# Kernel tuning notes

Hardware: AMD Instinct MI355X
Metric: run time of the kernel (lower is better)

Reference implementation:

```python
import jax, jax.numpy as jnp
import numpy as np

B, H, OUT = 16384, 1024, 128
W_SCALE = 0.03  # ~1/sqrt(H) so attention logits / softmax stay well-conditioned


def setup_inputs() -> dict:
    key = jax.random.key(0)
    ks = jax.random.split(key, 12)
    return {
        "f1": jax.random.normal(ks[0], (B, H), jnp.float32),
        "f2": jax.random.normal(ks[1], (B, H), jnp.float32),
        "f3": jax.random.normal(ks[2], (B, H), jnp.float32),
        "f4": jax.random.normal(ks[3], (B, H), jnp.float32),
        "Wq": jax.random.normal(ks[4], (H, H), jnp.float32) * W_SCALE,
        "bq": jax.random.normal(ks[5], (H,), jnp.float32) * W_SCALE,
        "Wk": jax.random.normal(ks[6], (H, H), jnp.float32) * W_SCALE,
        "bk": jax.random.normal(ks[7], (H,), jnp.float32) * W_SCALE,
        "Wv": jax.random.normal(ks[8], (H, H), jnp.float32) * W_SCALE,
        "bv": jax.random.normal(ks[9], (H,), jnp.float32) * W_SCALE,
        "Wfc": jax.random.normal(ks[10], (H, OUT), jnp.float32) * W_SCALE,
        "bfc": jax.random.normal(ks[11], (OUT,), jnp.float32) * W_SCALE,
    }


def reference(f1, f2, f3, f4, Wq, bq, Wk, bk, Wv, bv, Wfc, bfc):
    # Stack the 4 backbone features: z [B, 4, H]
    z = jnp.stack([f1, f2, f3, f4], axis=1)
    q = z @ Wq + bq            # [B, 4, H]
    k = z @ Wk + bk            # [B, 4, H]
    v = z @ Wv + bv            # [B, 4, H]
    # Tiny 4x4 self-attention over the 4 model-feature tokens
    score = jax.nn.softmax(jnp.einsum('bth,bsh->bts', q, k), axis=-1)  # [B,4,4]
    att = jnp.einsum('bts,bsh->bth', score, v)                          # [B,4,H]
    x = jnp.sum(att, axis=1)                                            # [B,H]
    out = jax.nn.softmax(x @ Wfc + bfc, axis=-1)                        # [B,OUT]
    return (x, out)
```

## Files before the change

kernel.cpp:

```cpp
#include <hip/hip_runtime.h>
#include <hip/hip_bf16.h>
#include <stdint.h>

#define B_SZ 16384
#define H_SZ 1024
#define OUT_SZ 128

typedef __attribute__((ext_vector_type(4))) float f32x4;
typedef __attribute__((ext_vector_type(8))) _Float16 h16x8;
typedef unsigned short u16;
typedef unsigned int u32;

__device__ __forceinline__ u16 f2h(float f) {
  union { _Float16 h; u16 u; } v; v.h = (_Float16)f; return v.u;
}
__device__ __forceinline__ float h2f(u16 u) {
  union { u16 u; _Float16 h; } v; v.u = u; return (float)v.h;
}
__device__ __forceinline__ u32 pk2(float a, float b) {
  return (u32)f2h(a) | ((u32)f2h(b) << 16);
}

__device__ __forceinline__ void gl_lds16(const void* g, void* l) {
  __builtin_amdgcn_global_load_lds(
      (const __attribute__((address_space(1))) u32*)g,
      (__attribute__((address_space(3))) u32*)l, 16, 0, 0);
}

template<int MODE>
__global__ __launch_bounds__(256, 4) void gemm_nt(
    const u16* __restrict__ Aptr, const u16* __restrict__ Bptr,
    int N, int K,
    float* __restrict__ ep_f, u16* __restrict__ ep_b,
    const float* __restrict__ ep_v,
    const float* zf0, const float* zf1, const float* zf2, const float* zf3)
{
  constexpr int BM = 128, BN = 128, BK = 32;
  __shared__ __align__(16) u16 sA[BM * BK];
  __shared__ __align__(16) u16 sB[BN * BK];
  const int tid  = threadIdx.x;
  const int wave = tid >> 6;
  const int lane = tid & 63;
  const int qd   = lane >> 4;
  const int c16  = lane & 15;
  const int bm0  = blockIdx.x * BM;
  const int bn0  = blockIdx.y * BN;
  const int wm   = (wave >> 1) * 64;
  const int wn   = (wave & 1) * 64;
  const size_t FBS = (size_t)B_SZ * H_SZ;

  f32x4 acc[4][4];
#pragma unroll
  for (int i = 0; i < 4; ++i)
#pragma unroll
    for (int j = 0; j < 4; ++j)
      acc[i][j] = (f32x4){0.f, 0.f, 0.f, 0.f};

  for (int k0 = 0; k0 < K; k0 += BK) {
#pragma unroll
    for (int i = 0; i < 2; ++i) {
      int slot = tid + i * 256;
      int r = slot >> 2, pp = slot & 3;
      int cc = pp ^ ((r >> 1) & 3);
      {
        int gm = bm0 + r;
        const u16* gp;
        if (MODE == 1)
          gp = Aptr + (size_t)(gm & 3) * FBS + (size_t)(gm >> 2) * H_SZ + (k0 + cc * 8);
        else
          gp = Aptr + (size_t)gm * K + (k0 + cc * 8);
        gl_lds16(gp, &sA[(size_t)(slot & ~63) * 8]);
      }
      {
        int gn = bn0 + r;
        const u16* gp = Bptr + (size_t)gn * K + (k0 + cc * 8);
        gl_lds16(gp, &sB[(size_t)(slot & ~63) * 8]);
      }
    }
    __syncthreads();
    h16x8 af[4], bfr[4];
#pragma unroll
    for (int im = 0; im < 4; ++im) {
      int m = wm + im * 16 + c16;
      int slot = m * 4 + (qd ^ ((m >> 1) & 3));
      af[im] = *(const h16x8*)&sA[slot * 8];
    }
#pragma unroll
    for (int in = 0; in < 4; ++in) {
      int n = wn + in * 16 + c16;
      int slot = n * 4 + (qd ^ ((n >> 1) & 3));
      bfr[in] = *(const h16x8*)&sB[slot * 8];
    }
#pragma unroll
    for (int im = 0; im < 4; ++im)
#pragma unroll
      for (int in = 0; in < 4; ++in)
        acc[im][in] = __builtin_amdgcn_mfma_f32_16x16x32_f16(af[im], bfr[in], acc[im][in], 0, 0, 0);
    __syncthreads();
  }

  if constexpr (MODE == 0) {
#pragma unroll
    for (int im = 0; im < 4; ++im)
#pragma unroll
      for (int in = 0; in < 4; ++in) {
        int n = bn0 + wn + in * 16 + c16;
#pragma unroll
        for (int r = 0; r < 4; ++r) {
          int m = bm0 + wm + im * 16 + qd * 4 + r;
          ep_b[(size_t)m * N + n] = f2h(acc[im][in][r]);
        }
      }
  } else if constexpr (MODE == 1) {
    const float* zf[4] = {zf0, zf1, zf2, zf3};
#pragma unroll
    for (int im = 0; im < 4; ++im) {
      int mrow = bm0 + wm + im * 16 + qd * 4;
      size_t b = (size_t)(mrow >> 2);
      float p[4][4];
#pragma unroll
      for (int r = 0; r < 4; ++r)
#pragma unroll
        for (int s = 0; s < 4; ++s) p[r][s] = 0.f;
#pragma unroll
      for (int in = 0; in < 4; ++in) {
        int n = bn0 + wn + in * 16 + c16;
        float akv = ep_v[n];
        float rv[4];
#pragma unroll
        for (int r = 0; r < 4; ++r) rv[r] = acc[im][in][r] + akv;
#pragma unroll
        for (int s = 0; s < 4; ++s) {
          float zv = zf[s][b * H_SZ + n];
#pragma unroll
          for (int r = 0; r < 4; ++r) p[r][s] += rv[r] * zv;
        }
      }
#pragma unroll
      for (int r = 0; r < 4; ++r)
#pragma unroll
        for (int s = 0; s < 4; ++s) {
          float v = p[r][s];
          v += __shfl_xor(v, 1);
          v += __shfl_xor(v, 2);
          v += __shfl_xor(v, 4);
          v += __shfl_xor(v, 8);
          if (c16 == 0) atomicAdd(&ep_f[b * 16 + r * 4 + s], v);
        }
    }
  } else if constexpr (MODE == 2) {
#pragma unroll
    for (int im = 0; im < 4; ++im)
#pragma unroll
      for (int in = 0; in < 4; ++in) {
        int n = bn0 + wn + in * 16 + c16;
        float bvv = 4.0f * ep_v[n];
#pragma unroll
        for (int r = 0; r < 4; ++r) {
          int m = bm0 + wm + im * 16 + qd * 4 + r;
          float v = acc[im][in][r] + bvv;
          ep_f[(size_t)m * H_SZ + n] = v;
          ep_b[(size_t)m * H_SZ + n] = f2h(v);
        }
      }
  } else {
#pragma unroll
    for (int im = 0; im < 4; ++im)
#pragma unroll
      for (int in = 0; in < 4; ++in) {
        int n = bn0 + wn + in * 16 + c16;
        float bc = ep_v[n];
#pragma unroll
        for (int r = 0; r < 4; ++r) {
          int m = bm0 + wm + im * 16 + qd * 4 + r;
          ep_f[(size_t)m * N + n] = acc[im][in][r] + bc;
        }
      }
  }
}

__global__ __launch_bounds__(256) void prep_weights(
    const float* __restrict__ Wq, const float* __restrict__ Wk,
    const float* __restrict__ Wv, const float* __restrict__ Wfc,
    const float* __restrict__ bq,
    u16* __restrict__ Wq16, u16* __restrict__ Wk16,
    u16* __restrict__ WvT, u16* __restrict__ WfcT,
    float* __restrict__ ak)
{
  __shared__ float t[32][33];
  int blk = blockIdx.x, tid = threadIdx.x;
  if (blk < 2048) {
    const float* src = (blk < 1024) ? Wq : Wk;
    u16* dst = (blk < 1024) ? Wq16 : Wk16;
    size_t i0 = (size_t)(blk & 1023) * 1024 + tid * 4;
    float4 v = *(const float4*)(src + i0);
    *(uint2*)(dst + i0) = make_uint2(pk2(v.x, v.y), pk2(v.z, v.w));
  } else if (blk < 3200) {
    int lx = tid & 31, ly = tid >> 5;
    if (blk < 3072) {
      int ti = blk - 2048;
      int tx = ti & 31, ty = ti >> 5;
#pragma unroll
      for (int k = 0; k < 4; ++k)
        t[ly + 8 * k][lx] = Wv[(size_t)(ty * 32 + ly + 8 * k) * 1024 + tx * 32 + lx];
      __syncthreads();
#pragma unroll
      for (int k = 0; k < 4; ++k)
        WvT[(size_t)(tx * 32 + ly + 8 * k) * 1024 + ty * 32 + lx] = f2h(t[lx][ly + 8 * k]);
    } else {
      int ti = blk - 3072;
      int tx = ti & 3, ty = ti >> 2;
#pragma unroll
      for (int k = 0; k < 4; ++k)
        t[ly + 8 * k][lx] = Wfc[(size_t)(ty * 32 + ly + 8 * k) * 128 + tx * 32 + lx];
      __syncthreads();
#pragma unroll
      for (int k = 0; k < 4; ++k)
        WfcT[(size_t)(tx * 32 + ly + 8 * k) * 1024 + ty * 32 + lx] = f2h(t[lx][ly + 8 * k]);
    }
  } else {
    int wave = tid >> 6, lane = tid & 63;
    int row = (blk - 3200) * 4 + wave;
    float s = 0.f;
    for (int i = lane; i < 1024; i += 64)
      s += Wk[(size_t)row * 1024 + i] * bq[i];
#pragma unroll
    for (int m = 1; m < 64; m <<= 1) s += __shfl_xor(s, m);
    if (lane == 0) ak[row] = s;
  }
}

__global__ __launch_bounds__(256) void convert4(
    const float* __restrict__ f1, const float* __restrict__ f2,
    const float* __restrict__ f3, const float* __restrict__ f4,
    u16* __restrict__ Zh)
{
  int a = blockIdx.x >> 13;
  const float* f = (a == 0) ? f1 : (a == 1) ? f2 : (a == 2) ? f3 : f4;
  size_t off = (size_t)(blockIdx.x & 8191) * 2048 + threadIdx.x * 8;
  float4 v0 = *(const float4*)(f + off);
  float4 v1 = *(const float4*)(f + off + 4);
  *(uint4*)(Zh + (size_t)a * B_SZ * H_SZ + off) =
      make_uint4(pk2(v0.x, v0.y), pk2(v0.z, v0.w), pk2(v1.x, v1.y), pk2(v1.z, v1.w));
}

__global__ __launch_bounds__(256) void softmax_g(
    const float* __restrict__ logits, const u16* __restrict__ Zh,
    u16* __restrict__ G)
{
  const size_t FBS = (size_t)B_SZ * H_SZ;
  int wave = threadIdx.x >> 6, lane = threadIdx.x & 63;
  size_t b = (size_t)blockIdx.x * 4 + wave;
  float l[16];
#pragma unroll
  for (int i = 0; i < 16; ++i) l[i] = logits[b * 16 + i];
  float w0 = 0, w1 = 0, w2 = 0, w3 = 0;
#pragma unroll
  for (int t = 0; t < 4; ++t) {
    float a0 = l[t * 4], a1 = l[t * 4 + 1], a2 = l[t * 4 + 2], a3 = l[t * 4 + 3];
    float mx = fmaxf(fmaxf(a0, a1), fmaxf(a2, a3));
    float e0 = __expf(a0 - mx), e1 = __expf(a1 - mx), e2 = __expf(a2 - mx), e3 = __expf(a3 - mx);
    float inv = 1.0f / (e0 + e1 + e2 + e3);
    w0 += e0 * inv; w1 += e1 * inv; w2 += e2 * inv; w3 += e3 * inv;
  }
#pragma unroll
  for (int ch = 0; ch < 2; ++ch) {
    size_t h0 = (size_t)lane * 8 + ch * 512;
    float g[8];
#pragma unroll
    for (int j = 0; j < 8; ++j) g[j] = 0.f;
#pragma unroll
    for (int s = 0; s < 4; ++s) {
      float ws = (s == 0) ? w0 : (s == 1) ? w1 : (s == 2) ? w2 : w3;
      uint4 zz = *(const uint4*)(Zh + (size_t)s * FBS + b * H_SZ + h0);
      u32 zs[4] = {zz.x, zz.y, zz.z, zz.w};
#pragma unroll
      for (int j = 0; j < 4; ++j) {
        g[2 * j]     += ws * h2f((u16)(zs[j] & 0xffffu));
        g[2 * j + 1] += ws * h2f((u16)(zs[j] >> 16));
      }
    }
    *(uint4*)(G + b * H_SZ + h0) =
        make_uint4(pk2(g[0], g[1]), pk2(g[2], g[3]), pk2(g[4], g[5]), pk2(g[6], g[7]));
  }
}

__global__ __launch_bounds__(256) void softmax_out(
    const float* __restrict__ L2, float* __restrict__ out)
{
  int wave = threadIdx.x >> 6, lane = threadIdx.x & 63;
  size_t row = (size_t)blockIdx.x * 4 + wave;
  float2 v = *(const float2*)(L2 + row * 128 + lane * 2);
  float mx = fmaxf(v.x, v.y);
#pragma unroll
  for (int m = 1; m < 64; m <<= 1) mx = fmaxf(mx, __shfl_xor(mx, m));
  float e0 = __expf(v.x - mx), e1 = __expf(v.y - mx);
  float s = e0 + e1;
#pragma unroll
  for (int m = 1; m < 64; m <<= 1) s += __shfl_xor(s, m);
  float inv = 1.0f / s;
  *(float2*)(out + row * 128 + lane * 2) = make_float2(e0 * inv, e1 * inv);
}

extern "C" void kernel_launch(void* const* d_in, const int* in_sizes, int n_in,
                              void* d_out, int out_size, void* d_ws, size_t ws_size,
                              hipStream_t stream)
{
  const float* f1  = (const float*)d_in[0];
  const float* f2  = (const float*)d_in[1];
  const float* f3  = (const float*)d_in[2];
  const float* f4  = (const float*)d_in[3];
  const float* Wq  = (const float*)d_in[4];
  const float* bq  = (const float*)d_in[5];
  const float* Wk  = (const float*)d_in[6];
  const float* Wv  = (const float*)d_in[8];
  const float* bv  = (const float*)d_in[9];
  const float* Wfc = (const float*)d_in[10];
  const float* bfc = (const float*)d_in[11];

  float* x_out = (float*)d_out;
  float* out2  = x_out + (size_t)B_SZ * H_SZ;

  const size_t BH = (size_t)B_SZ * H_SZ;
  const size_t HH = (size_t)H_SZ * H_SZ;
  char* w = (char*)d_ws;
  u16* Zh   = (u16*)w;  w += 4 * BH * sizeof(u16);
  u16* G    = (u16*)w;  w += BH * sizeof(u16);
  u16* Xh   = (u16*)w;  w += BH * sizeof(u16);
  u16* Wq16 = (u16*)w;  w += HH * 2;
  u16* Wk16 = (u16*)w;  w += HH * 2;
  u16* AT   = (u16*)w;  w += HH * 2;
  u16* WvT  = (u16*)w;  w += HH * 2;
  u16* WfcT = (u16*)w;  w += (size_t)OUT_SZ * H_SZ * 2;
  float* ak     = (float*)w;  w += H_SZ * sizeof(float);
  float* logits = (float*)w;  w += (size_t)B_SZ * 16 * sizeof(float);
  float* fcl    = (float*)w;  w += (size_t)B_SZ * OUT_SZ * sizeof(float);

  hipMemsetAsync(logits, 0, (size_t)B_SZ * 16 * sizeof(float), stream);
  prep_weights<<<3456, 256, 0, stream>>>(Wq, Wk, Wv, Wfc, bq,
      Wq16, Wk16, WvT, WfcT, ak);
  convert4<<<32768, 256, 0, stream>>>(f1, f2, f3, f4, Zh);
  gemm_nt<0><<<dim3(8, 8), 256, 0, stream>>>(
      Wk16, Wq16, 1024, 1024, nullptr, AT, nullptr,
      nullptr, nullptr, nullptr, nullptr);
  gemm_nt<1><<<dim3(512, 8), 256, 0, stream>>>(
      Zh, AT, 1024, 1024, logits, nullptr, ak, f1, f2, f3, f4);
  softmax_g<<<4096, 256, 0, stream>>>(logits, Zh, G);
  gemm_nt<2><<<dim3(128, 8), 256, 0, stream>>>(
      G, WvT, 1024, 1024, x_out, Xh, bv,
      nullptr, nullptr, nullptr, nullptr);
  gemm_nt<3><<<dim3(128, 1), 256, 0, stream>>>(
      Xh, WfcT, 128, 1024, fcl, nullptr, bfc,
      nullptr, nullptr, nullptr, nullptr);
  softmax_out<<<4096, 256, 0, stream>>>(fcl, out2);
}
```

Measured before the change: 784.8 us.

## Double-buffer GEMM LDS tiles and replace logit atomics with partial-sum buffer

The GEMM main loop now uses two LDS buffers per operand, issuing the next K-tile's global-to-LDS loads before computing on the current tile, so load latency can overlap MFMA work. The logits epilogue no longer uses atomicAdd into a zeroed buffer. Each of the 16 column groups writes its partial sum to a separate slot in a scratch area that aliases Xh, and softmax_g reduces those partials with shuffles. This removes the memset and the atomic contention, but doubles LDS use, which may lower occupancy. It also relies on Xh being free until the later GEMM writes it.

New measurement: 695.6 us. 11.4% less time.

```diff
diff --git a/kernel.cpp b/kernel.cpp
--- a/kernel.cpp
+++ b/kernel.cpp
@@ -36,8 +36,8 @@
     const float* zf0, const float* zf1, const float* zf2, const float* zf3)
 {
   constexpr int BM = 128, BN = 128, BK = 32;
-  __shared__ __align__(16) u16 sA[BM * BK];
-  __shared__ __align__(16) u16 sB[BN * BK];
+  __shared__ __align__(16) u16 sA[2][BM * BK];
+  __shared__ __align__(16) u16 sB[2][BN * BK];
   const int tid  = threadIdx.x;
   const int wave = tid >> 6;
   const int lane = tid & 63;
@@ -49,14 +49,7 @@
   const int wn   = (wave & 1) * 64;
   const size_t FBS = (size_t)B_SZ * H_SZ;
 
-  f32x4 acc[4][4];
-#pragma unroll
-  for (int i = 0; i < 4; ++i)
-#pragma unroll
-    for (int j = 0; j < 4; ++j)
-      acc[i][j] = (f32x4){0.f, 0.f, 0.f, 0.f};
-
-  for (int k0 = 0; k0 < K; k0 += BK) {
+  auto stage = [&](int buf, int k0) {
 #pragma unroll
     for (int i = 0; i < 2; ++i) {
       int slot = tid + i * 256;
@@ -69,27 +62,40 @@
           gp = Aptr + (size_t)(gm & 3) * FBS + (size_t)(gm >> 2) * H_SZ + (k0 + cc * 8);
         else
           gp = Aptr + (size_t)gm * K + (k0 + cc * 8);
-        gl_lds16(gp, &sA[(size_t)(slot & ~63) * 8]);
+        gl_lds16(gp, &sA[buf][(size_t)(slot & ~63) * 8]);
       }
       {
         int gn = bn0 + r;
         const u16* gp = Bptr + (size_t)gn * K + (k0 + cc * 8);
-        gl_lds16(gp, &sB[(size_t)(slot & ~63) * 8]);
-      }
-    }
-    __syncthreads();
+        gl_lds16(gp, &sB[buf][(size_t)(slot & ~63) * 8]);
+      }
+    }
+  };
+
+  f32x4 acc[4][4];
+#pragma unroll
+  for (int i = 0; i < 4; ++i)
+#pragma unroll
+    for (int j = 0; j < 4; ++j)
+      acc[i][j] = (f32x4){0.f, 0.f, 0.f, 0.f};
+
+  stage(0, 0);
+  __syncthreads();
+  int cur = 0;
+  for (int k0 = 0; k0 < K; k0 += BK) {
+    if (k0 + BK < K) stage(cur ^ 1, k0 + BK);
     h16x8 af[4], bfr[4];
 #pragma unroll
     for (int im = 0; im < 4; ++im) {
       int m = wm + im * 16 + c16;
       int slot = m * 4 + (qd ^ ((m >> 1) & 3));
-      af[im] = *(const h16x8*)&sA[slot * 8];
+      af[im] = *(const h16x8*)&sA[cur][slot * 8];
     }
 #pragma unroll
     for (int in = 0; in < 4; ++in) {
       int n = wn + in * 16 + c16;
       int slot = n * 4 + (qd ^ ((n >> 1) & 3));
-      bfr[in] = *(const h16x8*)&sB[slot * 8];
+      bfr[in] = *(const h16x8*)&sB[cur][slot * 8];
     }
 #pragma unroll
     for (int im = 0; im < 4; ++im)
@@ -97,6 +103,7 @@
       for (int in = 0; in < 4; ++in)
         acc[im][in] = __builtin_amdgcn_mfma_f32_16x16x32_f16(af[im], bfr[in], acc[im][in], 0, 0, 0);
     __syncthreads();
+    cur ^= 1;
   }
 
   if constexpr (MODE == 0) {
@@ -113,6 +120,7 @@
       }
   } else if constexpr (MODE == 1) {
     const float* zf[4] = {zf0, zf1, zf2, zf3};
+    const int yg = (int)blockIdx.y * 2 + (wn >> 6);
 #pragma unroll
     for (int im = 0; im < 4; ++im) {
       int mrow = bm0 + wm + im * 16 + qd * 4;
@@ -145,7 +153,7 @@
           v += __shfl_xor(v, 2);
           v += __shfl_xor(v, 4);
           v += __shfl_xor(v, 8);
-          if (c16 == 0) atomicAdd(&ep_f[b * 16 + r * 4 + s], v);
+          if (c16 == 0) ep_f[(b * 16 + (size_t)(r * 4 + s)) * 16 + yg] = v;
         }
     }
   } else if constexpr (MODE == 2) {
@@ -245,15 +253,19 @@
 }
 
 __global__ __launch_bounds__(256) void softmax_g(
-    const float* __restrict__ logits, const u16* __restrict__ Zh,
+    const float* __restrict__ pl, const u16* __restrict__ Zh,
     u16* __restrict__ G)
 {
   const size_t FBS = (size_t)B_SZ * H_SZ;
   int wave = threadIdx.x >> 6, lane = threadIdx.x & 63;
   size_t b = (size_t)blockIdx.x * 4 + wave;
+  float4 pv = *(const float4*)(pl + b * 256 + (size_t)lane * 4);
+  float part = pv.x + pv.y + pv.z + pv.w;
+  part += __shfl_xor(part, 1);
+  part += __shfl_xor(part, 2);
   float l[16];
 #pragma unroll
-  for (int i = 0; i < 16; ++i) l[i] = logits[b * 16 + i];
+  for (int i = 0; i < 16; ++i) l[i] = __shfl(part, i * 4);
   float w0 = 0, w1 = 0, w2 = 0, w3 = 0;
 #pragma unroll
   for (int t = 0; t < 4; ++t) {
@@ -332,11 +344,10 @@
   u16* AT   = (u16*)w;  w += HH * 2;
   u16* WvT  = (u16*)w;  w += HH * 2;
   u16* WfcT = (u16*)w;  w += (size_t)OUT_SZ * H_SZ * 2;
-  float* ak     = (float*)w;  w += H_SZ * sizeof(float);
-  float* logits = (float*)w;  w += (size_t)B_SZ * 16 * sizeof(float);
-  float* fcl    = (float*)w;  w += (size_t)B_SZ * OUT_SZ * sizeof(float);
-
-  hipMemsetAsync(logits, 0, (size_t)B_SZ * 16 * sizeof(float), stream);
+  float* ak  = (float*)w;  w += H_SZ * sizeof(float);
+  float* fcl = (float*)w;  w += (size_t)B_SZ * OUT_SZ * sizeof(float);
+  float* pl  = (float*)Xh;
+
   prep_weights<<<3456, 256, 0, stream>>>(Wq, Wk, Wv, Wfc, bq,
       Wq16, Wk16, WvT, WfcT, ak);
   convert4<<<32768, 256, 0, stream>>>(f1, f2, f3, f4, Zh);
@@ -344,8 +355,8 @@
       Wk16, Wq16, 1024, 1024, nullptr, AT, nullptr,
       nullptr, nullptr, nullptr, nullptr);
   gemm_nt<1><<<dim3(512, 8), 256, 0, stream>>>(
-      Zh, AT, 1024, 1024, logits, nullptr, ak, f1, f2, f3, f4);
-  softmax_g<<<4096, 256, 0, stream>>>(logits, Zh, G);
+      Zh, AT, 1024, 1024, pl, nullptr, ak, f1, f2, f3, f4);
+  softmax_g<<<4096, 256, 0, stream>>>(pl, Zh, G);
   gemm_nt<2><<<dim3(128, 8), 256, 0, stream>>>(
       G, WvT, 1024, 1024, x_out, Xh, bv,
       nullptr, nullptr, nullptr, nullptr);
```
